# Kernel optimization log

Measured on AMD Instinct MI355X. Metric: run time of the kernel, lower is better.

The kernel has to match this reference:

```python
import jax, jax.numpy as jnp
import numpy as np

B, S, D_IN, D, H = 2, 2048, 1024, 1024, 16
HD = D // H

def setup_inputs() -> dict:
    key = jax.random.key(0)
    k1, k2, k3 = jax.random.split(key, 3)
    # xavier_uniform-style scale for weights
    lim_qkv = float(np.sqrt(6.0 / (D_IN + 3 * D)))
    lim_o = float(np.sqrt(6.0 / (D + D)))
    return {
        "x": jax.random.normal(k1, (B, S, D_IN), dtype=jnp.float32),
        "w_qkv": jax.random.uniform(k2, (3 * D, D_IN), dtype=jnp.float32, minval=-lim_qkv, maxval=lim_qkv),
        "b_qkv": jnp.zeros((3 * D,), dtype=jnp.float32),
        "w_o": jax.random.uniform(k3, (D, D), dtype=jnp.float32, minval=-lim_o, maxval=lim_o),
        "b_o": jnp.zeros((D,), dtype=jnp.float32),
    }

def reference(x, w_qkv, b_qkv, w_o, b_o):
    b, s, _ = x.shape
    # QKV projection: [B,S,3D]
    qkv = jnp.einsum("bsd,ed->bse", x, w_qkv) + b_qkv
    # [B,S,H,3*HD] -> [B,H,S,3*HD]
    qkv = qkv.reshape(b, s, H, 3 * HD).transpose(0, 2, 1, 3)
    q, k, v = jnp.split(qkv, 3, axis=-1)  # each [B,H,S,HD]
    scale = 1.0 / jnp.sqrt(jnp.asarray(HD, dtype=q.dtype))
    logits = jnp.einsum("bhqd,bhkd->bhqk", q, k) * scale  # [B,H,S,S]
    attn = jax.nn.softmax(logits, axis=-1)
    vals = jnp.einsum("bhqk,bhkd->bhqd", attn, v)  # [B,H,S,HD]
    vals = vals.transpose(0, 2, 1, 3).reshape(b, s, D)
    return jnp.einsum("bsd,ed->bse", vals, w_o) + b_o
```

## Files before the change

### kernel.cpp

```cpp
#include <hip/hip_runtime.h>
#include <hip/hip_bf16.h>
#include <math.h>

#define BATCH 2
#define SLEN  2048
#define DIN   1024
#define DMODEL 1024
#define NHEAD 16
#define HD    64
#define E3    3072

typedef unsigned short us;
typedef _Float16 f16;
typedef __attribute__((ext_vector_type(8))) _Float16 f16x8;
typedef __attribute__((ext_vector_type(8))) unsigned short us8;
typedef __attribute__((ext_vector_type(4))) unsigned short us4;
typedef __attribute__((ext_vector_type(4))) float f32x4;
typedef __attribute__((ext_vector_type(16))) float f32x16;
typedef __attribute__((ext_vector_type(4))) unsigned int u32x4;

#define QSCALE 0.18033688011112042f

__device__ __forceinline__ us f16bits(float x) {
    const f16 h = (f16)x;
    return __builtin_bit_cast(us, h);
}

__device__ __forceinline__ unsigned int pkrtz(float a, float b) {
    return __builtin_bit_cast(unsigned int, __builtin_amdgcn_cvt_pkrtz(a, b));
}

__device__ __forceinline__ void plswap(unsigned int& a, unsigned int& b) {
    asm volatile("v_permlane32_swap_b32 %0, %1" : "+v"(a), "+v"(b));
}

__device__ __forceinline__ void barrier_raw() {
    asm volatile("s_barrier" ::: "memory");
}

#define GLL16(g, l)                                                                     \
    __builtin_amdgcn_global_load_lds((const __attribute__((address_space(1))) unsigned int*)(g), \
                                     (__attribute__((address_space(3))) unsigned int*)(l), 16, 0, 0)

__global__ __launch_bounds__(256) void cvt3_f16(
    const float* __restrict__ x, us* __restrict__ ox, int nx,
    const float* __restrict__ wq, us* __restrict__ owq, int nq,
    const float* __restrict__ wo, us* __restrict__ owo)
{
    int i = (blockIdx.x * 256 + threadIdx.x) * 8;
    const float* s;
    us* o;
    if (i < nx)           { s = x;  o = ox; }
    else if (i < nx + nq) { s = wq; o = owq; i -= nx; }
    else                  { s = wo; o = owo; i -= nx + nq; }
    const float4 f0 = *(const float4*)&s[i];
    const float4 f1 = *(const float4*)&s[i + 4];
    const float v[8] = {f0.x, f0.y, f0.z, f0.w, f1.x, f1.y, f1.z, f1.w};
    us8 h;
#pragma unroll
    for (int j = 0; j < 8; ++j) h[j] = f16bits(v[j]);
    *(us8*)&o[i] = h;
}

#define GBK 64
#define GNT (DIN / GBK)

template <int BN, bool QKV_OUT>
__global__ __launch_bounds__(256) void gemm_db(
    const us* __restrict__ Am, const us* __restrict__ Bm,
    const float* __restrict__ bias, void* __restrict__ Cout,
    int M, int N, int K)
{
    constexpr int NJ  = BN / 32;
    constexpr int BGL = BN / 32;
    __shared__ __align__(16) us ldsA[2 * 128 * 64];
    __shared__ __align__(16) us ldsB[2 * BN * 64];

    const int t    = threadIdx.x;
    const int lane = t & 63;
    const int w    = t >> 6;
    const int ml   = lane & 15;
    const int quad = lane >> 4;
    const int msk  = ml & 7;
    const int wm   = w >> 1;
    const int wn   = w & 1;

    const int nbx = N / BN;
    const int nwg = (M >> 7) * nbx;
    int wg = blockIdx.y * nbx + blockIdx.x;
    wg = (wg & 7) * (nwg >> 3) + (wg >> 3);
    const int m0 = (wg / nbx) * 128;
    const int n0 = (wg % nbx) * BN;

    const int r8  = lane >> 3;
    const int xsw = ((lane & 7) ^ r8) * 8;
    const us* pA = Am + (size_t)(m0 + w * 32 + r8) * K + xsw;
    const int brow = (BN == 128) ? w * 32 : w * 16;
    const us* pB = Bm + (size_t)(n0 + brow + r8) * K + xsw;

#define STG_A(d, kk) do { _Pragma("unroll") for (int g = 0; g < 4; ++g) \
    GLL16(pA + (size_t)(8 * g) * K + (kk), &ldsA[(d) * 8192 + w * 2048 + g * 512]); } while (0)
#define STG_B(d, kk) do { _Pragma("unroll") for (int g = 0; g < BGL; ++g) \
    GLL16(pB + (size_t)(8 * g) * K + (kk), &ldsB[(d) * (BN * 64) + brow * 64 + g * 512]); } while (0)

#define LDA(d, mi, ks) __builtin_bit_cast(f16x8, *(const us8*)&ldsA[(d) * 8192 + (wm * 64 + (mi) * 16 + ml) * 64 + (((quad ^ msk) ^ ((ks) << 2)) * 8)])
#define LDB(d, nj, ks) __builtin_bit_cast(f16x8, *(const us8*)&ldsB[(d) * (BN * 64) + (wn * (BN / 2) + (nj) * 16 + ml) * 64 + (((quad ^ msk) ^ ((ks) << 2)) * 8)])

#define WAIT_BGL() do { if constexpr (BN == 128) asm volatile("s_waitcnt vmcnt(4)" ::: "memory"); \
                        else                     asm volatile("s_waitcnt vmcnt(2)" ::: "memory"); } while (0)

    f32x4 acc[4][NJ];
#pragma unroll
    for (int i = 0; i < 4; ++i)
#pragma unroll
        for (int j = 0; j < NJ; ++j) {
            acc[i][j][0] = 0.f; acc[i][j][1] = 0.f; acc[i][j][2] = 0.f; acc[i][j][3] = 0.f;
        }

    STG_A(0, 0); STG_B(0, 0);
    STG_B(1, GBK);
    WAIT_BGL();
    barrier_raw();

    for (int tt = 0; tt < GNT; ++tt) {
        const int d = tt & 1, e = d ^ 1;

        if (tt + 1 < GNT) STG_A(e, (tt + 1) * GBK);
        f16x8 bf[2][NJ];
#pragma unroll
        for (int ks = 0; ks < 2; ++ks)
#pragma unroll
            for (int nj = 0; nj < NJ; ++nj)
                bf[ks][nj] = LDB(d, nj, ks);
        f16x8 a0[2][2];
#pragma unroll
        for (int mi = 0; mi < 2; ++mi) {
            a0[mi][0] = LDA(d, mi, 0);
            a0[mi][1] = LDA(d, mi, 1);
        }
        __builtin_amdgcn_s_setprio(1);
#pragma unroll
        for (int ks = 0; ks < 2; ++ks)
#pragma unroll
            for (int nj = 0; nj < NJ; ++nj)
#pragma unroll
                for (int mi = 0; mi < 2; ++mi)
                    acc[mi][nj] = __builtin_amdgcn_mfma_f32_16x16x32_f16(a0[mi][ks], bf[ks][nj], acc[mi][nj], 0, 0, 0);
        __builtin_amdgcn_s_setprio(0);
        barrier_raw();

        if (tt + 2 < GNT) STG_B(d, (tt + 2) * GBK);
        f16x8 a1[2][2];
#pragma unroll
        for (int mi = 0; mi < 2; ++mi) {
            a1[mi][0] = LDA(d, mi + 2, 0);
            a1[mi][1] = LDA(d, mi + 2, 1);
        }
        __builtin_amdgcn_s_setprio(1);
#pragma unroll
        for (int ks = 0; ks < 2; ++ks)
#pragma unroll
            for (int nj = 0; nj < NJ; ++nj)
#pragma unroll
                for (int mi = 0; mi < 2; ++mi)
                    acc[mi + 2][nj] = __builtin_amdgcn_mfma_f32_16x16x32_f16(a1[mi][ks], bf[ks][nj], acc[mi + 2][nj], 0, 0, 0);
        __builtin_amdgcn_s_setprio(0);

        if (tt + 2 < GNT)      WAIT_BGL();
        else if (tt + 1 < GNT) asm volatile("s_waitcnt vmcnt(0)" ::: "memory");
        barrier_raw();
    }

    float bj[NJ], cs[NJ];
#pragma unroll
    for (int nj = 0; nj < NJ; ++nj) {
        const int col = n0 + wn * (BN / 2) + nj * 16 + ml;
        bj[nj] = bias[col];
        cs[nj] = (QKV_OUT && (col % 192) < 64) ? QSCALE : 1.0f;
    }
#pragma unroll
    for (int mi = 0; mi < 4; ++mi) {
#pragma unroll
        for (int r = 0; r < 4; ++r) {
            const size_t rowoff = (size_t)(m0 + wm * 64 + mi * 16 + quad * 4 + r) * N;
#pragma unroll
            for (int nj = 0; nj < NJ; ++nj) {
                const int col = n0 + wn * (BN / 2) + nj * 16 + ml;
                const float v = (acc[mi][nj][r] + bj[nj]) * cs[nj];
                if (QKV_OUT) ((us*)Cout)[rowoff + col] = f16bits(v);
                else         ((float*)Cout)[rowoff + col] = v;
            }
        }
    }
#undef STG_A
#undef STG_B
#undef LDA
#undef LDB
#undef WAIT_BGL
}

#define ABQ 128
#define ACH 64
#define NCH (SLEN / ACH)
#define NCH2 (NCH / 2)
#define LQA 72
#define OSTR 68

__global__ __launch_bounds__(512, 2) void attn_mfma(
    const us* __restrict__ qkvh, us* __restrict__ vals)
{
    __shared__ __align__(16) us smem[36864];

    const int t    = threadIdx.x;
    const int lane = t & 63;
    const int w    = t >> 6;
    const int sp   = w >> 2;
    const int wq4  = w & 3;
    const int t2   = t & 255;
    const int m32  = lane & 31;
    const int half = lane >> 5;

    const int wg  = blockIdx.x;
    const int s9  = wg >> 3;
    const int bh  = ((s9 >> 4) << 3) | (wg & 7);
    const int b   = bh >> 4;
    const int h   = bh & 15;
    const int q0  = (s9 & 15) * ABQ;

    const size_t base = (size_t)b * SLEN * E3;
    const int qoff = h * 192;

    const int krA = t2 >> 2;
    const int ksA = (t2 & 3) * 16;
    const int k2  = t2 & 31;
    const int d0v = (t2 >> 5) * 8;

    us* const Kb0 = smem + sp * 4608;
    us* const Kb1 = smem + 9216 + sp * 4608;
    us* const Vb0 = smem + 18432 + sp * 4608;
    us* const Vb1 = smem + 27648 + sp * 4608;
    const int cg0 = sp * NCH2;

    us8 kk0, kk1, vv0, vv1;
#define LOADKV(cgi) do { \
    const us* gK = &qkvh[base + (size_t)((cgi) * ACH + krA) * E3 + qoff + 64 + ksA]; \
    kk0 = *(const us8*)gK; kk1 = *(const us8*)(gK + 8); \
    const us* gV = &qkvh[base + (size_t)((cgi) * ACH + 2 * k2) * E3 + qoff + 128 + d0v]; \
    vv0 = *(const us8*)gV; vv1 = *(const us8*)(gV + E3); } while (0)

    LOADKV(cg0);
    {
        const int row = t >> 2;
        const int c0q = (t & 3) * 16;
        const us* g = &qkvh[base + (size_t)(q0 + row) * E3 + qoff + c0q];
        *(us8*)&smem[row * LQA + c0q]     = *(const us8*)g;
        *(us8*)&smem[row * LQA + c0q + 8] = *(const us8*)(g + 8);
    }
    __syncthreads();

    f16x8 aq[4];
#pragma unroll
    for (int s = 0; s < 4; ++s)
        aq[s] = __builtin_bit_cast(f16x8, *(const us8*)&smem[(wq4 * 32 + m32) * LQA + half * 8 + 16 * s]);
    __syncthreads();

    *(us8*)&Kb0[krA * LQA + ksA]     = kk0;
    *(us8*)&Kb0[krA * LQA + ksA + 8] = kk1;
#pragma unroll
    for (int j = 0; j < 8; ++j) {
        const unsigned int pv = (unsigned int)vv0[j] | ((unsigned int)vv1[j] << 16);
        *(unsigned int*)&Vb0[(d0v + j) * LQA + 2 * k2] = pv;
    }
    LOADKV(cg0 + 1);
    __syncthreads();

    f32x16 O[2];
#pragma unroll
    for (int dt = 0; dt < 2; ++dt)
#pragma unroll
        for (int r = 0; r < 16; ++r) O[dt][r] = 0.f;
    float lp[2] = {0.f, 0.f};

    for (int c = 0; c < NCH2; ++c) {
        us* const Krd = (c & 1) ? Kb1 : Kb0;
        us* const Vrd = (c & 1) ? Vb1 : Vb0;
        us* const Kwr = (c & 1) ? Kb0 : Kb1;
        us* const Vwr = (c & 1) ? Vb0 : Vb1;

        if (c + 1 < NCH2) {
            *(us8*)&Kwr[krA * LQA + ksA]     = kk0;
            *(us8*)&Kwr[krA * LQA + ksA + 8] = kk1;
#pragma unroll
            for (int j = 0; j < 8; ++j) {
                const unsigned int pv = (unsigned int)vv0[j] | ((unsigned int)vv1[j] << 16);
                *(unsigned int*)&Vwr[(d0v + j) * LQA + 2 * k2] = pv;
            }
        }
        if (c + 2 < NCH2) LOADKV(cg0 + c + 2);

        f16x8 pf[4];
#pragma unroll
        for (int kt = 0; kt < 2; ++kt) {
            f32x16 z;
#pragma unroll
            for (int r = 0; r < 16; ++r) z[r] = 0.f;
            __builtin_amdgcn_s_setprio(1);
#pragma unroll
            for (int s = 0; s < 4; ++s) {
                const f16x8 ak = __builtin_bit_cast(f16x8, *(const us8*)&Krd[(kt * 32 + m32) * LQA + half * 8 + 16 * s]);
                z = __builtin_amdgcn_mfma_f32_32x32x16_f16(ak, aq[s], z, 0, 0, 0);
            }
            __builtin_amdgcn_s_setprio(0);
            {
                float p[8];
#pragma unroll
                for (int r = 0; r < 8; ++r) {
                    p[r] = __builtin_amdgcn_exp2f(z[r]);
                    lp[r & 1] += p[r];
                }
                unsigned int a0 = pkrtz(p[0], p[1]), a1 = pkrtz(p[2], p[3]);
                unsigned int b0 = pkrtz(p[4], p[5]), b1 = pkrtz(p[6], p[7]);
                plswap(a0, b0); plswap(a1, b1);
                pf[2 * kt] = __builtin_bit_cast(f16x8, (u32x4){a0, a1, b0, b1});
            }
            {
                float p[8];
#pragma unroll
                for (int r = 0; r < 8; ++r) {
                    p[r] = __builtin_amdgcn_exp2f(z[8 + r]);
                    lp[r & 1] += p[r];
                }
                unsigned int e0 = pkrtz(p[0], p[1]), e1 = pkrtz(p[2], p[3]);
                unsigned int f0 = pkrtz(p[4], p[5]), f1 = pkrtz(p[6], p[7]);
                plswap(e0, f0); plswap(e1, f1);
                pf[2 * kt + 1] = __builtin_bit_cast(f16x8, (u32x4){e0, e1, f0, f1});
            }
        }

        __builtin_amdgcn_s_setprio(1);
#pragma unroll
        for (int dt = 0; dt < 2; ++dt) {
#pragma unroll
            for (int s = 0; s < 4; ++s) {
                const f16x8 av = __builtin_bit_cast(f16x8, *(const us8*)&Vrd[(dt * 32 + m32) * LQA + half * 8 + 16 * s]);
                O[dt] = __builtin_amdgcn_mfma_f32_32x32x16_f16(av, pf[s], O[dt], 0, 0, 0);
            }
        }
        __builtin_amdgcn_s_setprio(0);

        __syncthreads();
    }

    const float lpart = lp[0] + lp[1];
    const float l = lpart + __shfl_xor(lpart, 32);
    const int ql = wq4 * 32 + m32;

    __syncthreads();
    float* const Osc = (float*)smem;
    float* const lsc = Osc + ABQ * OSTR;

    if (sp == 1) {
#pragma unroll
        for (int dt = 0; dt < 2; ++dt) {
#pragma unroll
            for (int g = 0; g < 4; ++g) {
                const f32x4 o4 = {O[dt][g * 4], O[dt][g * 4 + 1], O[dt][g * 4 + 2], O[dt][g * 4 + 3]};
                *(f32x4*)&Osc[ql * OSTR + dt * 32 + 8 * g + 4 * half] = o4;
            }
        }
        if (half == 0) lsc[ql] = l;
    }
    __syncthreads();
    if (sp == 0) {
        const float rl = 1.0f / (l + lsc[ql]);
        const int sq = q0 + ql;
        const size_t rowbase = (size_t)(b * SLEN + sq) * DMODEL + h * HD;
#pragma unroll
        for (int dt = 0; dt < 2; ++dt) {
#pragma unroll
            for (int g = 0; g < 4; ++g) {
                const f32x4 part = *(const f32x4*)&Osc[ql * OSTR + dt * 32 + 8 * g + 4 * half];
                us4 o4;
#pragma unroll
                for (int r2 = 0; r2 < 4; ++r2)
                    o4[r2] = f16bits((O[dt][g * 4 + r2] + part[r2]) * rl);
                *(us4*)&vals[rowbase + dt * 32 + 8 * g + 4 * half] = o4;
            }
        }
    }
#undef LOADKV
}

extern "C" void kernel_launch(void* const* d_in, const int* in_sizes, int n_in,
                              void* d_out, int out_size, void* d_ws, size_t ws_size,
                              hipStream_t stream) {
    const float* x     = (const float*)d_in[0];
    const float* w_qkv = (const float*)d_in[1];
    const float* b_qkv = (const float*)d_in[2];
    const float* w_o   = (const float*)d_in[3];
    const float* b_o   = (const float*)d_in[4];
    float* out = (float*)d_out;

    const int M   = BATCH * SLEN;
    const int XN  = M * DIN;
    const int WQN = E3 * DIN;
    const int WON = DMODEL * DMODEL;
    const size_t QKVN = (size_t)BATCH * SLEN * E3;

    us* qkvh = (us*)d_ws;
    us* xh   = qkvh + QKVN;
    us* wq   = xh + XN;
    us* wo   = wq + WQN;

    cvt3_f16<<<dim3((XN + WQN + WON) / 2048), 256, 0, stream>>>(
        x, xh, XN, w_qkv, wq, WQN, w_o, wo);

    gemm_db<128, true><<<dim3(E3 / 128, M / 128), 256, 0, stream>>>(
        xh, wq, b_qkv, qkvh, M, E3, DIN);

    us* vals = xh;
    attn_mfma<<<dim3((SLEN / ABQ) * BATCH * NHEAD), 512, 0, stream>>>(qkvh, vals);

    gemm_db<64, false><<<dim3(DMODEL / 64, M / 128), 256, 0, stream>>>(
        vals, wo, b_o, out, M, DMODEL, DMODEL);
}
```

Baseline: 189.0 us.

## Add 256x256-tile 512-thread GEMM for QKV projection and widen output GEMM tile

Adds a new GEMM kernel that uses 256x256 output tiles with 8 waves, a double-buffered LDS pipeline with staggered A/B prefetch, XOR-swizzled LDS, s_setprio around the MFMA blocks, and an XCD-aware workgroup remap. The QKV projection now uses this kernel, which should cut global and LDS traffic per FLOP through greater reuse. The output projection switches from a 64-wide to a 128-wide N tile. The QKV grid drops to 192 blocks of one workgroup per CU, which risks underfilling the 256 CUs and adds register pressure from 128 accumulators per thread.

```diff
diff --git a/kernel.cpp b/kernel.cpp
--- a/kernel.cpp
+++ b/kernel.cpp
@@ -62,6 +62,135 @@
     *(us8*)&o[i] = h;
 }
 
+#define G2BK 64
+
+template <bool QKV_OUT>
+__global__ __launch_bounds__(512, 1) void gemm256_f16(
+    const us* __restrict__ Am, const us* __restrict__ Bm,
+    const float* __restrict__ bias, void* __restrict__ Cout,
+    int M, int N, int K)
+{
+    __shared__ __align__(16) us ldsA[2 * 256 * 64];
+    __shared__ __align__(16) us ldsB[2 * 256 * 64];
+
+    const int t    = threadIdx.x;
+    const int lane = t & 63;
+    const int w    = t >> 6;
+    const int ml   = lane & 15;
+    const int quad = lane >> 4;
+    const int msk  = ml & 7;
+    const int wm   = w >> 2;
+    const int wn   = w & 3;
+    const int GNT  = K / G2BK;
+
+    const int nbx = N >> 8;
+    const int nwg = (M >> 8) * nbx;
+    int wg = blockIdx.y * nbx + blockIdx.x;
+    wg = (wg & 7) * (nwg >> 3) + (wg >> 3);
+    const int m0 = (wg / nbx) * 256;
+    const int n0 = (wg % nbx) * 256;
+
+    const int r8  = lane >> 3;
+    const int xsw = ((lane & 7) ^ r8) * 8;
+    const us* pA = Am + (size_t)(m0 + w * 32 + r8) * K + xsw;
+    const us* pB = Bm + (size_t)(n0 + w * 32 + r8) * K + xsw;
+
+#define STG_A(d, kk) do { _Pragma("unroll") for (int g = 0; g < 4; ++g) \
+    GLL16(pA + (size_t)(8 * g) * K + (kk), &ldsA[(d) * 16384 + w * 2048 + g * 512]); } while (0)
+#define STG_B(d, kk) do { _Pragma("unroll") for (int g = 0; g < 4; ++g) \
+    GLL16(pB + (size_t)(8 * g) * K + (kk), &ldsB[(d) * 16384 + w * 2048 + g * 512]); } while (0)
+
+#define LDA(d, mi, ks) __builtin_bit_cast(f16x8, *(const us8*)&ldsA[(d) * 16384 + (wm * 128 + (mi) * 16 + ml) * 64 + (((quad ^ msk) ^ ((ks) << 2)) * 8)])
+#define LDB(d, nj, ks) __builtin_bit_cast(f16x8, *(const us8*)&ldsB[(d) * 16384 + (wn * 64 + (nj) * 16 + ml) * 64 + (((quad ^ msk) ^ ((ks) << 2)) * 8)])
+
+    f32x4 acc[8][4];
+#pragma unroll
+    for (int i = 0; i < 8; ++i)
+#pragma unroll
+        for (int j = 0; j < 4; ++j) {
+            acc[i][j][0] = 0.f; acc[i][j][1] = 0.f; acc[i][j][2] = 0.f; acc[i][j][3] = 0.f;
+        }
+
+    STG_A(0, 0); STG_B(0, 0);
+    STG_B(1, G2BK);
+    asm volatile("s_waitcnt vmcnt(4)" ::: "memory");
+    barrier_raw();
+
+    for (int tt = 0; tt < GNT; ++tt) {
+        const int d = tt & 1, e = d ^ 1;
+
+        if (tt + 1 < GNT) STG_A(e, (tt + 1) * G2BK);
+        f16x8 bf[2][4];
+#pragma unroll
+        for (int ks = 0; ks < 2; ++ks)
+#pragma unroll
+            for (int nj = 0; nj < 4; ++nj)
+                bf[ks][nj] = LDB(d, nj, ks);
+        f16x8 af[4][2];
+#pragma unroll
+        for (int mi = 0; mi < 4; ++mi) {
+            af[mi][0] = LDA(d, mi, 0);
+            af[mi][1] = LDA(d, mi, 1);
+        }
+        __builtin_amdgcn_s_setprio(1);
+#pragma unroll
+        for (int ks = 0; ks < 2; ++ks)
+#pragma unroll
+            for (int nj = 0; nj < 4; ++nj)
+#pragma unroll
+                for (int mi = 0; mi < 4; ++mi)
+                    acc[mi][nj] = __builtin_amdgcn_mfma_f32_16x16x32_f16(af[mi][ks], bf[ks][nj], acc[mi][nj], 0, 0, 0);
+        __builtin_amdgcn_s_setprio(0);
+        barrier_raw();
+
+        if (tt + 2 < GNT) STG_B(d, (tt + 2) * G2BK);
+#pragma unroll
+        for (int mi = 0; mi < 4; ++mi) {
+            af[mi][0] = LDA(d, mi + 4, 0);
+            af[mi][1] = LDA(d, mi + 4, 1);
+        }
+        __builtin_amdgcn_s_setprio(1);
+#pragma unroll
+        for (int ks = 0; ks < 2; ++ks)
+#pragma unroll
+            for (int nj = 0; nj < 4; ++nj)
+#pragma unroll
+                for (int mi = 0; mi < 4; ++mi)
+                    acc[mi + 4][nj] = __builtin_amdgcn_mfma_f32_16x16x32_f16(af[mi][ks], bf[ks][nj], acc[mi + 4][nj], 0, 0, 0);
+        __builtin_amdgcn_s_setprio(0);
+
+        if (tt + 2 < GNT)      asm volatile("s_waitcnt vmcnt(4)" ::: "memory");
+        else if (tt + 1 < GNT) asm volatile("s_waitcnt vmcnt(0)" ::: "memory");
+        barrier_raw();
+    }
+
+    float bj[4], cs[4];
+#pragma unroll
+    for (int nj = 0; nj < 4; ++nj) {
+        const int col = n0 + wn * 64 + nj * 16 + ml;
+        bj[nj] = bias[col];
+        cs[nj] = (QKV_OUT && (col % 192) < 64) ? QSCALE : 1.0f;
+    }
+#pragma unroll
+    for (int mi = 0; mi < 8; ++mi) {
+#pragma unroll
+        for (int r = 0; r < 4; ++r) {
+            const size_t rowoff = (size_t)(m0 + wm * 128 + mi * 16 + quad * 4 + r) * N;
+#pragma unroll
+            for (int nj = 0; nj < 4; ++nj) {
+                const int col = n0 + wn * 64 + nj * 16 + ml;
+                const float v = (acc[mi][nj][r] + bj[nj]) * cs[nj];
+                if (QKV_OUT) ((us*)Cout)[rowoff + col] = f16bits(v);
+                else         ((float*)Cout)[rowoff + col] = v;
+            }
+        }
+    }
+#undef STG_A
+#undef STG_B
+#undef LDA
+#undef LDB
+}
+
 #define GBK 64
 #define GNT (DIN / GBK)
 
@@ -415,12 +544,12 @@
     cvt3_f16<<<dim3((XN + WQN + WON) / 2048), 256, 0, stream>>>(
         x, xh, XN, w_qkv, wq, WQN, w_o, wo);
 
-    gemm_db<128, true><<<dim3(E3 / 128, M / 128), 256, 0, stream>>>(
+    gemm256_f16<true><<<dim3(E3 / 256, M / 256), 512, 0, stream>>>(
         xh, wq, b_qkv, qkvh, M, E3, DIN);
 
     us* vals = xh;
     attn_mfma<<<dim3((SLEN / ABQ) * BATCH * NHEAD), 512, 0, stream>>>(qkvh, vals);
 
-    gemm_db<64, false><<<dim3(DMODEL / 64, M / 128), 256, 0, stream>>>(
+    gemm_db<128, false><<<dim3(DMODEL / 128, M / 128), 256, 0, stream>>>(
         vals, wo, b_o, out, M, DMODEL, DMODEL);
 }
```

Measured after the change: 187.4 us. About the same (-0.9%).
